# Optimization experiments

Measured on AMD Instinct MI355X. Metric: run time of the kernel, lower is better.

The kernel has to match this reference:

```python
import jax, jax.numpy as jnp
import numpy as np
import math

B, S, D, H = 4, 1024, 1024, 16
HD = D // H  # 64
DFF = 4 * D
LN_EPS = 1e-5

def setup_inputs() -> dict:
    key = jax.random.key(0)
    ks = jax.random.split(key, 24)
    sd = lambda fi, fo: 1.0 / math.sqrt(fi)
    def lin(k, fi, fo):
        k1, k2 = jax.random.split(k)
        w = jax.random.uniform(k1, (fi, fo), jnp.float32, -sd(fi, fo), sd(fi, fo))
        b = jax.random.uniform(k2, (fo,), jnp.float32, -sd(fi, fo), sd(fi, fo))
        return w, b
    x = jax.random.normal(ks[0], (B, S, D), jnp.float32)
    Wk, bk = lin(ks[1], D, D)
    Wq, bq = lin(ks[2], D, D)
    Wv, bv = lin(ks[3], D, D)
    # per-head projections stacked over heads: [H, D, HD]
    def head_lin(k):
        kk = jax.random.split(k, H)
        ws, bs = zip(*[lin(kk[h], D, HD) for h in range(H)])
        return jnp.stack(ws), jnp.stack(bs)
    Whq, bhq = head_lin(ks[4])
    Whk, bhk = head_lin(ks[5])
    Whv, bhv = head_lin(ks[6])
    Wo, bo = lin(ks[7], D, D)
    W1, b1 = lin(ks[8], D, DFF)
    W2, b2 = lin(ks[9], DFF, D)
    gamma = jnp.ones((D,), jnp.float32)
    beta = jnp.zeros((D,), jnp.float32)
    return dict(x=x, Wk=Wk, bk=bk, Wq=Wq, bq=bq, Wv=Wv, bv=bv,
                Whq=Whq, bhq=bhq, Whk=Whk, bhk=bhk, Whv=Whv, bhv=bhv,
                Wo=Wo, bo=bo, W1=W1, b1=b1, W2=W2, b2=b2,
                gamma=gamma, beta=beta)

def _layer_norm(x, gamma, beta):
    mu = jnp.mean(x, axis=-1, keepdims=True)
    var = jnp.mean(jnp.square(x - mu), axis=-1, keepdims=True)
    return (x - mu) * jax.lax.rsqrt(var + LN_EPS) * gamma + beta

def reference(x, Wk, bk, Wq, bq, Wv, bv, Whq, bhq, Whk, bhk, Whv, bhv,
              Wo, bo, W1, b1, W2, b2, gamma, beta):
    # outer projections; NOTE: forward passes (k, q, v) into MHA, so the
    # MHA 'Q' stream is k_proj(x), 'K' stream is q_proj(x), 'V' is v_proj(x)
    ko = x @ Wk + bk
    qo = x @ Wq + bq
    vo = x @ Wv + bv
    # per-head projections (batched over heads): [B,H,S,HD]
    q = jnp.einsum('bsd,hde->bhse', ko, Whq) + bhq[None, :, None, :]
    k = jnp.einsum('bsd,hde->bhse', qo, Whk) + bhk[None, :, None, :]
    v = jnp.einsum('bsd,hde->bhse', vo, Whv) + bhv[None, :, None, :]
    # NOTE: original scales by sqrt(d_model), not sqrt(head_dim)
    scores = jnp.einsum('bhse,bhte->bhst', q, k) / math.sqrt(D)
    w = jax.nn.softmax(scores, axis=-1)
    o = jnp.einsum('bhst,bhte->bhse', w, v)         # [B,H,S,HD]
    o = o.transpose(0, 2, 1, 3).reshape(B, S, D)    # concat heads
    attn = o @ Wo + bo
    # dropout is identity in eval; shared LayerNorm after both residuals
    r1 = _layer_norm(x + attn, gamma, beta)
    ff = jax.nn.gelu(r1 @ W1 + b1, approximate=False) @ W2 + b2
    out = _layer_norm(r1 + ff, gamma, beta)
    return out
```

## Files before the change

kernel.cpp:

```cpp
#include <hip/hip_runtime.h>
#include <cstdint>
#include <cstddef>

#define D_MODEL 1024
#define SEQ 1024
#define BATCH 4
#define NHEAD 16
#define HDIM 64
#define ROWS (BATCH*SEQ)

typedef unsigned short u16;
typedef __attribute__((ext_vector_type(4))) unsigned short u16x4;
typedef __attribute__((ext_vector_type(8))) unsigned short u16x8;
typedef __attribute__((ext_vector_type(8))) __bf16 bf16x8v;
typedef __attribute__((ext_vector_type(4))) float f32x4;

__device__ inline u16 f2bf(float f){
  union{float f; unsigned u;} c; c.f = f;
  unsigned r = c.u + 0x7FFFu + ((c.u>>16)&1u);
  return (u16)(r>>16);
}
__device__ inline float bf2f(u16 s){
  union{unsigned u; float f;} c; c.u = ((unsigned)s)<<16; return c.f;
}
__device__ inline float gelu_f(float x){ return 0.5f*x*(1.f+erff(x*0.7071067811865475f)); }

__device__ __forceinline__ void gload_lds16(const void* g, void* l){
  __builtin_amdgcn_global_load_lds(
    (const __attribute__((address_space(1))) unsigned int*)g,
    (__attribute__((address_space(3))) unsigned int*)l, 16, 0, 0);
}

struct C4 { const float* src[4]; u16* dst[4]; };
__global__ __launch_bounds__(256) void convert4(C4 p){
  int bid = blockIdx.x;
  int which, off;
  if (bid < 4096){ which = 0; off = bid; }
  else { which = 1 + ((bid-4096) >> 10); off = (bid-4096) & 1023; }
  size_t idx = (size_t)off*256 + threadIdx.x;
  f32x4 v = *(const f32x4*)(p.src[which] + idx*4);
  u16x4 o = { f2bf(v.x), f2bf(v.y), f2bf(v.z), f2bf(v.w) };
  *(u16x4*)(p.dst[which] + idx*4) = o;
}

struct T3 { const float* W[3]; u16* WT[3]; };
__global__ __launch_bounds__(256) void transpose3(T3 p){
  __shared__ float tile[32][33];
  int bid = blockIdx.x;
  int which, bx, by, K, N;
  if (bid < 1024){ which=0; K=1024; N=1024; bx=bid&31;  by=bid>>5; }
  else if (bid < 5120){ int i=bid-1024; which=1; K=1024; N=4096; bx=i&127; by=i>>7; }
  else { int i=bid-5120; which=2; K=4096; N=1024; bx=i&31; by=i>>5; }
  const float* W = p.W[which];
  u16* WT = p.WT[which];
  int n0 = bx*32, k0 = by*32;
  int tx = threadIdx.x & 31, ty = threadIdx.x >> 5;
  #pragma unroll
  for (int i=0;i<4;i++){
    int r = ty + i*8;
    tile[r][tx] = W[(size_t)(k0+r)*N + n0 + tx];
  }
  __syncthreads();
  #pragma unroll
  for (int i=0;i<4;i++){
    int r = ty + i*8;
    WT[(size_t)(n0+r)*K + k0 + tx] = f2bf(tile[tx][r]);
  }
}

struct H3 { const float* src[3]; u16* dst[3]; };
__global__ __launch_bounds__(256) void head_transpose3(H3 p){
  __shared__ float tile[32][33];
  int z = blockIdx.z; int which = z >> 4; int h = z & 15;
  const float* Wh = p.src[which];
  u16* WT = p.dst[which];
  int d0 = blockIdx.x*32, e0 = blockIdx.y*32;
  int tx = threadIdx.x & 31, ty = threadIdx.x >> 5;
  #pragma unroll
  for (int i=0;i<4;i++){
    int r = ty + i*8;
    tile[r][tx] = Wh[(size_t)h*D_MODEL*HDIM + (size_t)(d0+r)*HDIM + e0 + tx];
  }
  __syncthreads();
  #pragma unroll
  for (int i=0;i<4;i++){
    int r = ty + i*8;
    WT[(size_t)(h*HDIM + e0 + r)*D_MODEL + d0 + tx] = f2bf(tile[tx][r]);
  }
}

__global__ __launch_bounds__(64) void bias_comb(
  const float* bk, const float* bq, const float* bv,
  const float* Whq, const float* Whk, const float* Whv,
  const float* bhq, const float* bhk, const float* bhv, float* bc)
{
  int blk = blockIdx.x; int which = blk >> 4; int h = blk & 15; int e = threadIdx.x;
  const float* bvec = (which==0) ? bk : (which==1) ? bq : bv;
  const float* Wh   = (which==0) ? Whq : (which==1) ? Whk : Whv;
  const float* bh   = (which==0) ? bhq : (which==1) ? bhk : bhv;
  float s = bh[h*HDIM + e];
  const float* w = Wh + (size_t)h*D_MODEL*HDIM + e;
  for (int d=0; d<D_MODEL; ++d) s += bvec[d] * w[(size_t)d*HDIM];
  bc[which*1024 + h*HDIM + e] = s;
}

__global__ __launch_bounds__(512,1) void gemm256_8p(
  const u16* __restrict__ A, const u16* __restrict__ BT, const float* __restrict__ bias,
  u16* __restrict__ outB, int N, int K, int mode, int act)
{
  __shared__ __align__(16) u16 As[2][2][128*64];
  __shared__ __align__(16) u16 Bs[2][2][128*64];
  int t = threadIdx.x, lane = t&63, wid = t>>6;
  int wr = wid>>2, wc = wid&3;
  int fr = lane&15, kg = lane>>4;
  int gx = gridDim.x;
  int bid = blockIdx.y*gx + blockIdx.x;
  int nwg = gx*gridDim.y;
  int cpx = nwg>>3;
  int sw = (bid&7)*cpx + (bid>>3);
  int tc = sw % gx, tr = sw / gx;

  const u16* Abase = A  + (size_t)tr*256*K;
  const u16* Bbase = BT + (size_t)tc*256*K;
  int srow = lane>>3, sch8 = lane&7;

  f32x4 acc[8][4];
  #pragma unroll
  for (int m=0;m<8;m++)
    #pragma unroll
    for (int n=0;n<4;n++) acc[m][n] = (f32x4)0.f;

  bf16x8v af[2][4], bv0[2][2], bv1[2][2];

  #define STAGE_A8(buf,h,kt) { _Pragma("unroll") for (int li=0;li<2;li++){ \
    int sr = (wid*2+li)*8 + srow; \
    int gr = ((sr>>6)<<7) + (h)*64 + (sr&63); \
    int sc = sch8 ^ (sr&7); \
    gload_lds16(Abase + (size_t)gr*K + (size_t)(kt)*64 + sc*8, &As[buf][h][(wid*2+li)*512]); } }
  #define STAGE_B8(buf,h,kt) { _Pragma("unroll") for (int li=0;li<2;li++){ \
    int sr = (wid*2+li)*8 + srow; \
    int gc = ((sr>>5)<<6) + (h)*32 + (sr&31); \
    int sc = sch8 ^ (sr&7); \
    gload_lds16(Bbase + (size_t)gc*K + (size_t)(kt)*64 + sc*8, &Bs[buf][h][(wid*2+li)*512]); } }
  #define STAGE_ALL(buf,kt) { STAGE_A8(buf,0,kt); STAGE_B8(buf,0,kt); STAGE_B8(buf,1,kt); STAGE_A8(buf,1,kt); }
  #define LDA8(buf,h) { _Pragma("unroll") for (int ks=0;ks<2;ks++) _Pragma("unroll") for (int mf=0;mf<4;mf++){ \
    int r = wr*64 + mf*16 + fr; \
    af[ks][mf] = *(const bf16x8v*)&As[buf][h][r*64 + (((kg+4*ks)^(r&7)))*8]; } }
  #define LDB8(buf,h,dst) { _Pragma("unroll") for (int ks=0;ks<2;ks++) _Pragma("unroll") for (int nf=0;nf<2;nf++){ \
    int r = wc*32 + nf*16 + fr; \
    dst[ks][nf] = *(const bf16x8v*)&Bs[buf][h][r*64 + (((kg+4*ks)^(r&7)))*8]; } }
  #define MM8(mq,nq,bv) { asm volatile("s_waitcnt lgkmcnt(0)" ::: "memory"); \
    __builtin_amdgcn_s_setprio(1); \
    _Pragma("unroll") for (int ks=0;ks<2;ks++) _Pragma("unroll") for (int mf=0;mf<4;mf++) _Pragma("unroll") for (int nf=0;nf<2;nf++) \
      acc[(mq)*4+mf][(nq)*2+nf] = __builtin_amdgcn_mfma_f32_16x16x32_bf16(af[ks][mf], bv[ks][nf], acc[(mq)*4+mf][(nq)*2+nf], 0,0,0); \
    __builtin_amdgcn_s_setprio(0); }
  #define BAR asm volatile("s_barrier" ::: "memory")

  int NT = K >> 6;
  STAGE_ALL(0,0);

  for (int kt=0; kt<NT; ++kt){
    int buf = kt&1, nb = buf^1;
    if (kt+1 < NT){
      STAGE_ALL(nb, kt+1);
      asm volatile("s_waitcnt vmcnt(8)" ::: "memory");
    } else {
      asm volatile("s_waitcnt vmcnt(0)" ::: "memory");
    }
    BAR;
    LDA8(buf,0); LDB8(buf,0,bv0); MM8(0,0,bv0);
    LDB8(buf,1,bv1);              MM8(0,1,bv1);
    LDA8(buf,1);                  MM8(1,1,bv1);
                                  MM8(1,0,bv0);
  }

  int crow0 = tr*256 + wr*128;
  int ccol0 = tc*256 + wc*64;
  #pragma unroll
  for (int n=0;n<4;n++){
    int col = ccol0 + n*16 + fr;
    float bv = bias[col];
    #pragma unroll
    for (int m=0;m<8;m++){
      int rbase = crow0 + m*16 + kg*4;
      #pragma unroll
      for (int i=0;i<4;i++){
        float v = acc[m][n][i] + bv;
        if (act) v = gelu_f(v);
        int row = rbase + i;
        if (mode == 1){
          outB[(size_t)row*N + col] = f2bf(v);
        } else {
          int panel = col >> 10, c1 = col & 1023;
          if (panel < 2)
            outB[(size_t)panel*((size_t)ROWS*1024) + (size_t)row*1024 + c1] = f2bf(v);
          else {
            int b = row >> 10, s = row & 1023;
            int hh = c1 >> 6, e = c1 & 63;
            outB[(size_t)2*((size_t)ROWS*1024) + (((size_t)((b*NHEAD+hh)*HDIM+e))<<10) + s] = f2bf(v);
          }
        }
      }
    }
  }
}

__device__ __forceinline__ void stage128(u16 (*As)[4096], u16 (*Bs)[4096], int b,
  const u16* Ab, const u16* Bb, int Kstride, int kt, int wid, int rr, int sch)
{
  #pragma unroll
  for (int c=0;c<2;c++){
    int reg = c*4 + wid;
    int row = reg*16 + rr;
    gload_lds16(Ab + (size_t)row*Kstride + kt*32 + sch*8, &As[b][reg*512]);
  }
  #pragma unroll
  for (int c=0;c<2;c++){
    int reg = c*4 + wid;
    int row = reg*16 + rr;
    gload_lds16(Bb + (size_t)row*Kstride + kt*32 + sch*8, &Bs[b][reg*512]);
  }
}

__device__ __forceinline__ void gemm128_core(u16 (*As)[4096], u16 (*Bs)[4096],
  const u16* __restrict__ A, const u16* __restrict__ BT, const float* __restrict__ bias,
  float* __restrict__ outF, u16* __restrict__ outB,
  int N, int Kstride, int kofs, int Ksub, int mode, int act, int addbias)
{
  int t = threadIdx.x, lane = t&63, wid = t>>6;
  int wr = wid>>1, wc = wid&1;
  int fr = lane&15, kg = lane>>4;
  int gx = gridDim.x;
  int bid = blockIdx.y*gx + blockIdx.x;
  int nwg = gx*gridDim.y;
  int cpx = nwg >> 3;
  int sw = (bid&7)*cpx + (bid>>3);
  int tc = sw % gx, tr = sw / gx;

  const u16* Ab = A  + (size_t)tr*128*Kstride + kofs;
  const u16* Bb = BT + (size_t)tc*128*Kstride + kofs;
  int rr = lane>>2, cc = lane&3;
  int sch = cc ^ ((rr>>1)&3);

  f32x4 acc[4][4];
  #pragma unroll
  for (int m=0;m<4;m++)
    #pragma unroll
    for (int n=0;n<4;n++) acc[m][n] = (f32x4)0.f;

  int NT = Ksub >> 5;

  stage128(As, Bs, 0, Ab, Bb, Kstride, 0, wid, rr, sch);
  stage128(As, Bs, 1, Ab, Bb, Kstride, 1, wid, rr, sch);
  int buf = 0;
  for (int kt=0; kt<NT; ++kt){
    if (kt+2 < NT){
      int nb = buf+2; if (nb>=3) nb-=3;
      stage128(As, Bs, nb, Ab, Bb, Kstride, kt+2, wid, rr, sch);
      asm volatile("s_waitcnt vmcnt(8)" ::: "memory");
    } else if (kt+1 < NT){
      asm volatile("s_waitcnt vmcnt(4)" ::: "memory");
    } else {
      asm volatile("s_waitcnt vmcnt(0)" ::: "memory");
    }
    asm volatile("s_barrier" ::: "memory");
    bf16x8v af[4], bfv[4];
    #pragma unroll
    for (int m=0;m<4;m++){
      int r = wr*64 + m*16 + fr;
      af[m] = *(const bf16x8v*)&As[buf][r*32 + (kg ^ ((r>>1)&3))*8];
    }
    #pragma unroll
    for (int n=0;n<4;n++){
      int r = wc*64 + n*16 + fr;
      bfv[n] = *(const bf16x8v*)&Bs[buf][r*32 + (kg ^ ((r>>1)&3))*8];
    }
    #pragma unroll
    for (int m=0;m<4;m++)
      #pragma unroll
      for (int n=0;n<4;n++)
        acc[m][n] = __builtin_amdgcn_mfma_f32_16x16x32_bf16(af[m], bfv[n], acc[m][n], 0,0,0);
    if (kt+1 < NT)
      asm volatile("s_barrier" ::: "memory");
    buf += 1; if (buf >= 3) buf = 0;
  }

  int crow0 = tr*128 + wr*64;
  int ccol0 = tc*128 + wc*64;
  #pragma unroll
  for (int n=0;n<4;n++){
    int col = ccol0 + n*16 + fr;
    float bv = addbias ? bias[col] : 0.f;
    #pragma unroll
    for (int m=0;m<4;m++){
      int rbase = crow0 + m*16 + kg*4;
      #pragma unroll
      for (int i=0;i<4;i++){
        float v = acc[m][n][i] + bv;
        if (act) v = gelu_f(v);
        int row = rbase + i;
        if (mode == 1){
          outB[(size_t)row*N + col] = f2bf(v);
        } else {
          outF[(size_t)row*1024 + col] = v;
        }
      }
    }
  }
}

__global__ __launch_bounds__(256) void g_gemm_sk(
  const u16* A, const u16* BT, const float* bias, float* outBase, int K)
{
  __shared__ __align__(16) u16 As[3][4096];
  __shared__ __align__(16) u16 Bs[3][4096];
  int z = blockIdx.z;
  int Ksub = K >> 1;
  gemm128_core(As, Bs, A, BT, bias, outBase + (size_t)z*ROWS*1024, nullptr,
               1024, K, z*Ksub, Ksub, 3, 0, z==0);
}

struct B3 { const u16* A[3]; const u16* BT[3]; u16* Cb[3]; };
__global__ __launch_bounds__(256) void g_gemm_b3(B3 p, const float* bias){
  __shared__ __align__(16) u16 As[3][4096];
  __shared__ __align__(16) u16 Bs[3][4096];
  int z = blockIdx.z;
  gemm128_core(As, Bs, p.A[z], p.BT[z], bias, nullptr, p.Cb[z],
               1024, 1024, 0, 1024, 1, 0, 0);
}

__global__ __launch_bounds__(256) void attn_mfma(const u16* __restrict__ Q, const u16* __restrict__ Km,
                                                 const u16* __restrict__ Vt, u16* __restrict__ O)
{
  __shared__ __align__(16) u16 Ks[64*64];
  __shared__ __align__(16) u16 Vs[64*64];
  __shared__ __align__(16) u16 Ps[4][16*64];
  int t = threadIdx.x, lane = t & 63, wid = t >> 6;
  int fr = lane & 15, kg = lane >> 4;
  int qt = blockIdx.x, h = blockIdx.y, b = blockIdx.z;
  const size_t qkbase = ((size_t)b*SEQ)*D_MODEL + (size_t)h*HDIM;
  const size_t vtb = ((size_t)(b*NHEAD + h))*HDIM*SEQ;

  int qrow = qt*64 + wid*16 + fr;
  bf16x8v aq0 = *(const bf16x8v*)(Q + qkbase + (size_t)qrow*D_MODEL + kg*8);
  bf16x8v aq1 = *(const bf16x8v*)(Q + qkbase + (size_t)qrow*D_MODEL + 32 + kg*8);

  f32x4 Oacc[4];
  #pragma unroll
  for (int n=0;n<4;n++) Oacc[n] = (f32x4)0.f;
  float m_run[4], l_run[4];
  #pragma unroll
  for (int i=0;i<4;i++){ m_run[i] = -3e38f; l_run[i] = 0.f; }

  int srow = lane >> 3;
  int sch  = (lane & 7) ^ srow;
  int x7 = fr & 7;
  const float CS = 0.03125f * 1.4426950408889634f;
  u16* Pw = &Ps[wid][0];

  for (int kt = 0; kt < SEQ/64; ++kt){
    __syncthreads();
    #pragma unroll
    for (int c=0;c<2;c++){
      int r0 = (wid*2 + c)*8;
      int rowk = r0 + srow;
      gload_lds16(Km + qkbase + (size_t)(kt*64 + rowk)*D_MODEL + sch*8, &Ks[r0*64]);
      gload_lds16(Vt + vtb + (size_t)rowk*SEQ + kt*64 + sch*8, &Vs[r0*64]);
    }
    asm volatile("s_waitcnt vmcnt(0)" ::: "memory");
    __syncthreads();

    f32x4 s4[4];
    #pragma unroll
    for (int n=0;n<4;n++){
      int r = n*16 + fr;
      bf16x8v k0 = *(const bf16x8v*)&Ks[r*64 + ((kg  ) ^ x7)*8];
      bf16x8v k1 = *(const bf16x8v*)&Ks[r*64 + ((4+kg) ^ x7)*8];
      f32x4 z = (f32x4)0.f;
      z = __builtin_amdgcn_mfma_f32_16x16x32_bf16(aq0, k0, z, 0,0,0);
      s4[n] = __builtin_amdgcn_mfma_f32_16x16x32_bf16(aq1, k1, z, 0,0,0);
    }
    #pragma unroll
    for (int n=0;n<4;n++) s4[n] *= CS;

    float mI[4];
    #pragma unroll
    for (int i=0;i<4;i++)
      mI[i] = fmaxf(fmaxf(s4[0][i], s4[1][i]), fmaxf(s4[2][i], s4[3][i]));
    #pragma unroll
    for (int off=1; off<16; off<<=1){
      #pragma unroll
      for (int i=0;i<4;i++) mI[i] = fmaxf(mI[i], __shfl_xor(mI[i], off));
    }
    float g = -3e38f;
    #pragma unroll
    for (int i=0;i<4;i++) g = fmaxf(g, mI[i] - m_run[i]);
    if (__any(g > 8.f)){
      #pragma unroll
      for (int i=0;i<4;i++){
        float mn = fmaxf(m_run[i], mI[i]);
        float sc = exp2f(m_run[i] - mn);
        m_run[i] = mn;
        l_run[i] *= sc;
        #pragma unroll
        for (int n=0;n<4;n++) Oacc[n][i] *= sc;
      }
    }
    float ls[4] = {0.f,0.f,0.f,0.f};
    #pragma unroll
    for (int n=0;n<4;n++){
      int chunk = n*2 + (fr>>3);
      #pragma unroll
      for (int i=0;i<4;i++){
        float pv = exp2f(s4[n][i] - m_run[i]);
        ls[i] += pv;
        int row = kg*4 + i;
        Pw[row*64 + (chunk ^ (row&7))*8 + (fr&7)] = f2bf(pv);
      }
    }
    #pragma unroll
    for (int off=1; off<16; off<<=1){
      #pragma unroll
      for (int i=0;i<4;i++) ls[i] += __shfl_xor(ls[i], off);
    }
    #pragma unroll
    for (int i=0;i<4;i++) l_run[i] += ls[i];
    asm volatile("s_waitcnt lgkmcnt(0)" ::: "memory");

    bf16x8v ap0 = *(const bf16x8v*)&Pw[fr*64 + ((kg  ) ^ x7)*8];
    bf16x8v ap1 = *(const bf16x8v*)&Pw[fr*64 + ((4+kg) ^ x7)*8];
    #pragma unroll
    for (int n2=0;n2<4;n2++){
      int r = n2*16 + fr;
      bf16x8v v0 = *(const bf16x8v*)&Vs[r*64 + ((kg  ) ^ x7)*8];
      bf16x8v v1 = *(const bf16x8v*)&Vs[r*64 + ((4+kg) ^ x7)*8];
      Oacc[n2] = __builtin_amdgcn_mfma_f32_16x16x32_bf16(ap0, v0, Oacc[n2], 0,0,0);
      Oacc[n2] = __builtin_amdgcn_mfma_f32_16x16x32_bf16(ap1, v1, Oacc[n2], 0,0,0);
    }
  }

  float inv[4];
  #pragma unroll
  for (int i=0;i<4;i++) inv[i] = 1.f / l_run[i];
  #pragma unroll
  for (int n2=0;n2<4;n2++){
    #pragma unroll
    for (int i=0;i<4;i++){
      int row = qt*64 + wid*16 + kg*4 + i;
      O[qkbase + (size_t)row*D_MODEL + n2*16 + fr] = f2bf(Oacc[n2][i]*inv[i]);
    }
  }
}

__global__ __launch_bounds__(256) void ln_sum3(const float* __restrict__ A, const float* __restrict__ B,
   const float* __restrict__ C, const float* __restrict__ gamma, const float* __restrict__ beta,
   float* __restrict__ Of, u16* __restrict__ Ob)
{
  int row = blockIdx.x, t = threadIdx.x;
  size_t base = (size_t)row*D_MODEL + t*4;
  f32x4 v = *(const f32x4*)(A + base);
  v += *(const f32x4*)(B + base);
  v += *(const f32x4*)(C + base);
  float s = v.x+v.y+v.z+v.w;
  float q = v.x*v.x+v.y*v.y+v.z*v.z+v.w*v.w;
  #pragma unroll
  for (int off=1; off<64; off<<=1){ s += __shfl_xor(s,off); q += __shfl_xor(q,off); }
  __shared__ float red[8];
  int wid = t>>6;
  if ((t&63)==0){ red[wid] = s; red[wid+4] = q; }
  __syncthreads();
  s = red[0]+red[1]+red[2]+red[3];
  q = red[4]+red[5]+red[6]+red[7];
  float mu = s*(1.f/1024.f);
  float var = q*(1.f/1024.f) - mu*mu;
  float rs = rsqrtf(var + 1e-5f);
  f32x4 g4 = *(const f32x4*)(gamma + t*4);
  f32x4 b4 = *(const f32x4*)(beta + t*4);
  f32x4 o;
  o.x = (v.x-mu)*rs*g4.x + b4.x;
  o.y = (v.y-mu)*rs*g4.y + b4.y;
  o.z = (v.z-mu)*rs*g4.z + b4.z;
  o.w = (v.w-mu)*rs*g4.w + b4.w;
  if (Of) *(f32x4*)(Of + base) = o;
  if (Ob){
    u16x4 ob = { f2bf(o.x), f2bf(o.y), f2bf(o.z), f2bf(o.w) };
    *(u16x4*)(Ob + base) = ob;
  }
}

extern "C" void kernel_launch(void* const* d_in, const int* in_sizes, int n_in,
                              void* d_out, int out_size, void* d_ws, size_t ws_size,
                              hipStream_t stream)
{
  const float* x    = (const float*)d_in[0];
  const float* Wk   = (const float*)d_in[1];
  const float* bk   = (const float*)d_in[2];
  const float* Wq   = (const float*)d_in[3];
  const float* bq   = (const float*)d_in[4];
  const float* Wv   = (const float*)d_in[5];
  const float* bv   = (const float*)d_in[6];
  const float* Whq  = (const float*)d_in[7];
  const float* bhq  = (const float*)d_in[8];
  const float* Whk  = (const float*)d_in[9];
  const float* bhk  = (const float*)d_in[10];
  const float* Whv  = (const float*)d_in[11];
  const float* bhv  = (const float*)d_in[12];
  const float* Wo   = (const float*)d_in[13];
  const float* bo   = (const float*)d_in[14];
  const float* W1   = (const float*)d_in[15];
  const float* b1   = (const float*)d_in[16];
  const float* W2   = (const float*)d_in[17];
  const float* b2   = (const float*)d_in[18];
  const float* gamma= (const float*)d_in[19];
  const float* beta = (const float*)d_in[20];

  char* ws = (char*)d_ws;
  const size_t MB_ = 1024*1024;
  u16* Wkb  = (u16*)(ws + 0*MB_);
  u16* Wqb  = (u16*)(ws + 2*MB_);
  u16* Wvb  = (u16*)(ws + 4*MB_);
  u16* WhqT = (u16*)(ws + 6*MB_);
  u16* WhkT = (u16*)(ws + 8*MB_);
  u16* WhvT = (u16*)(ws + 10*MB_);
  u16* WoT  = (u16*)(ws + 12*MB_);
  u16* W1T  = (u16*)(ws + 14*MB_);
  u16* W2T  = (u16*)(ws + 22*MB_);
  u16* xb   = (u16*)(ws + 30*MB_);
  u16* WcT  = (u16*)(ws + 38*MB_);
  float* bc = (float*)(ws + 44*MB_);
  u16* qb   = (u16*)(ws + 46*MB_);
  u16* kb   = (u16*)(ws + 54*MB_);
  u16* vt   = (u16*)(ws + 62*MB_);
  u16* Ob   = (u16*)(ws + 70*MB_);
  float* Pa = (float*)(ws + 78*MB_);
  float* Pb = (float*)(ws + 94*MB_);
  float* r1f = (float*)(ws + 110*MB_);
  u16*  r1b  = (u16*)(ws + 38*MB_);
  u16*  ff1b = (u16*)(ws + 46*MB_);

  dim3 tb(256);

  C4 cv; cv.src[0]=x; cv.src[1]=Wk; cv.src[2]=Wq; cv.src[3]=Wv;
  cv.dst[0]=xb; cv.dst[1]=Wkb; cv.dst[2]=Wqb; cv.dst[3]=Wvb;
  convert4<<<dim3(4096+3072), tb, 0, stream>>>(cv);
  H3 hh; hh.src[0]=Whq; hh.src[1]=Whk; hh.src[2]=Whv;
  hh.dst[0]=WhqT; hh.dst[1]=WhkT; hh.dst[2]=WhvT;
  head_transpose3<<<dim3(32,2,48), tb, 0, stream>>>(hh);
  T3 tt; tt.W[0]=Wo; tt.W[1]=W1; tt.W[2]=W2;
  tt.WT[0]=WoT; tt.WT[1]=W1T; tt.WT[2]=W2T;
  transpose3<<<dim3(9216), tb, 0, stream>>>(tt);
  bias_comb<<<dim3(48), dim3(64), 0, stream>>>(bk,bq,bv, Whq,Whk,Whv, bhq,bhk,bhv, bc);

  B3 cmb;
  cmb.A[0]=WhqT; cmb.A[1]=WhkT; cmb.A[2]=WhvT;
  cmb.BT[0]=Wkb; cmb.BT[1]=Wqb; cmb.BT[2]=Wvb;
  cmb.Cb[0]=WcT; cmb.Cb[1]=WcT+1048576; cmb.Cb[2]=WcT+2097152;
  g_gemm_b3<<<dim3(8,8,3), tb, 0, stream>>>(cmb, bk);

  gemm256_8p<<<dim3(12,16), dim3(512), 0, stream>>>(xb, WcT, bc, qb, 3072, 1024, 2, 0);

  attn_mfma<<<dim3(16,16,4), tb, 0, stream>>>(qb, kb, vt, Ob);

  g_gemm_sk<<<dim3(8,32,2), tb, 0, stream>>>(Ob, WoT, bo, Pa, 1024);
  ln_sum3<<<dim3(4096), tb, 0, stream>>>(x, Pa, Pb, gamma, beta, r1f, r1b);
  gemm256_8p<<<dim3(16,16), dim3(512), 0, stream>>>(r1b, W1T, b1, ff1b, 4096, 1024, 1, 1);
  g_gemm_sk<<<dim3(8,32,2), tb, 0, stream>>>(ff1b, W2T, b2, Pa, 4096);
  ln_sum3<<<dim3(4096), tb, 0, stream>>>(r1f, Pa, Pb, gamma, beta, (float*)d_out, nullptr);

  (void)in_sizes; (void)n_in; (void)out_size; (void)ws_size;
}
```

Baseline: 333.0 us.

## Merge weight prep kernels, parallelize bias combine, defer softmax row-sum reduction

Folds the input conversion, weight transposes and per-head transposes into one prep_all launch, removing two kernel launches. bias_comb now uses 256 threads, splitting the 1024-long dot product into four segments reduced through shared memory. In attention, the per-tile cross-lane shuffle reduction of the softmax denominator moves out of the loop to a single reduction at the end, and P is rounded to bf16 with a cheaper round-half-up conversion that gives slightly different results on ties.

```diff
diff --git a/kernel.cpp b/kernel.cpp
--- a/kernel.cpp
+++ b/kernel.cpp
@@ -20,6 +20,10 @@
   unsigned r = c.u + 0x7FFFu + ((c.u>>16)&1u);
   return (u16)(r>>16);
 }
+__device__ inline u16 f2bf_fast(float f){
+  union{float f; unsigned u;} c; c.f = f;
+  return (u16)((c.u + 0x8000u)>>16);
+}
 __device__ inline float bf2f(u16 s){
   union{unsigned u; float f;} c; c.u = ((unsigned)s)<<16; return c.f;
 }
@@ -31,28 +35,39 @@
     (__attribute__((address_space(3))) unsigned int*)l, 16, 0, 0);
 }
 
-struct C4 { const float* src[4]; u16* dst[4]; };
-__global__ __launch_bounds__(256) void convert4(C4 p){
+struct PrepAll {
+  const float* conv_src[4]; u16* conv_dst[4];
+  const float* tr_src[3];   u16* tr_dst[3];
+  const float* h_src[3];    u16* h_dst[3];
+};
+__global__ __launch_bounds__(256) void prep_all(PrepAll p){
   int bid = blockIdx.x;
-  int which, off;
-  if (bid < 4096){ which = 0; off = bid; }
-  else { which = 1 + ((bid-4096) >> 10); off = (bid-4096) & 1023; }
-  size_t idx = (size_t)off*256 + threadIdx.x;
-  f32x4 v = *(const f32x4*)(p.src[which] + idx*4);
-  u16x4 o = { f2bf(v.x), f2bf(v.y), f2bf(v.z), f2bf(v.w) };
-  *(u16x4*)(p.dst[which] + idx*4) = o;
-}
-
-struct T3 { const float* W[3]; u16* WT[3]; };
-__global__ __launch_bounds__(256) void transpose3(T3 p){
+  if (bid < 7168){
+    int which, off;
+    if (bid < 4096){ which = 0; off = bid; }
+    else { which = 1 + ((bid-4096) >> 10); off = (bid-4096) & 1023; }
+    size_t idx = (size_t)off*256 + threadIdx.x;
+    f32x4 v = *(const f32x4*)(p.conv_src[which] + idx*4);
+    u16x4 o = { f2bf(v.x), f2bf(v.y), f2bf(v.z), f2bf(v.w) };
+    *(u16x4*)(p.conv_dst[which] + idx*4) = o;
+    return;
+  }
   __shared__ float tile[32][33];
-  int bid = blockIdx.x;
-  int which, bx, by, K, N;
-  if (bid < 1024){ which=0; K=1024; N=1024; bx=bid&31;  by=bid>>5; }
-  else if (bid < 5120){ int i=bid-1024; which=1; K=1024; N=4096; bx=i&127; by=i>>7; }
-  else { int i=bid-5120; which=2; K=4096; N=1024; bx=i&31; by=i>>5; }
-  const float* W = p.W[which];
-  u16* WT = p.WT[which];
+  bid -= 7168;
+  const float* W; u16* WT; int K, N, bx, by;
+  if (bid < 1024){ W=p.tr_src[0]; WT=p.tr_dst[0]; K=1024; N=1024; bx=bid&31; by=bid>>5; }
+  else if (bid < 5120){ int i=bid-1024; W=p.tr_src[1]; WT=p.tr_dst[1]; K=1024; N=4096; bx=i&127; by=i>>7; }
+  else if (bid < 9216){ int i=bid-5120; W=p.tr_src[2]; WT=p.tr_dst[2]; K=4096; N=1024; bx=i&31; by=i>>5; }
+  else {
+    int i = bid - 9216;
+    int which = i >> 10;
+    int j = i & 1023;
+    int h = j >> 6;
+    int d0t = (j>>1)&31, e0t = j&1;
+    W  = p.h_src[which] + (size_t)h*D_MODEL*HDIM;
+    WT = p.h_dst[which] + (size_t)h*HDIM*D_MODEL;
+    K = 1024; N = 64; bx = e0t; by = d0t;
+  }
   int n0 = bx*32, k0 = by*32;
   int tx = threadIdx.x & 31, ty = threadIdx.x >> 5;
   #pragma unroll
@@ -68,40 +83,26 @@
   }
 }
 
-struct H3 { const float* src[3]; u16* dst[3]; };
-__global__ __launch_bounds__(256) void head_transpose3(H3 p){
-  __shared__ float tile[32][33];
-  int z = blockIdx.z; int which = z >> 4; int h = z & 15;
-  const float* Wh = p.src[which];
-  u16* WT = p.dst[which];
-  int d0 = blockIdx.x*32, e0 = blockIdx.y*32;
-  int tx = threadIdx.x & 31, ty = threadIdx.x >> 5;
-  #pragma unroll
-  for (int i=0;i<4;i++){
-    int r = ty + i*8;
-    tile[r][tx] = Wh[(size_t)h*D_MODEL*HDIM + (size_t)(d0+r)*HDIM + e0 + tx];
-  }
-  __syncthreads();
-  #pragma unroll
-  for (int i=0;i<4;i++){
-    int r = ty + i*8;
-    WT[(size_t)(h*HDIM + e0 + r)*D_MODEL + d0 + tx] = f2bf(tile[tx][r]);
-  }
-}
-
-__global__ __launch_bounds__(64) void bias_comb(
+__global__ __launch_bounds__(256) void bias_comb(
   const float* bk, const float* bq, const float* bv,
   const float* Whq, const float* Whk, const float* Whv,
   const float* bhq, const float* bhk, const float* bhv, float* bc)
 {
-  int blk = blockIdx.x; int which = blk >> 4; int h = blk & 15; int e = threadIdx.x;
+  int blk = blockIdx.x; int which = blk >> 4; int h = blk & 15;
+  int e = threadIdx.x & 63, seg = threadIdx.x >> 6;
   const float* bvec = (which==0) ? bk : (which==1) ? bq : bv;
   const float* Wh   = (which==0) ? Whq : (which==1) ? Whk : Whv;
   const float* bh   = (which==0) ? bhq : (which==1) ? bhk : bhv;
-  float s = bh[h*HDIM + e];
   const float* w = Wh + (size_t)h*D_MODEL*HDIM + e;
-  for (int d=0; d<D_MODEL; ++d) s += bvec[d] * w[(size_t)d*HDIM];
-  bc[which*1024 + h*HDIM + e] = s;
+  float s = 0.f;
+  for (int d = seg*256; d < seg*256+256; ++d) s += bvec[d] * w[(size_t)d*HDIM];
+  __shared__ float red[256];
+  red[threadIdx.x] = s;
+  __syncthreads();
+  if (seg == 0){
+    s = red[e] + red[e+64] + red[e+128] + red[e+192] + bh[h*HDIM + e];
+    bc[which*1024 + h*HDIM + e] = s;
+  }
 }
 
 __global__ __launch_bounds__(512,1) void gemm256_8p(
@@ -406,25 +407,17 @@
         for (int n=0;n<4;n++) Oacc[n][i] *= sc;
       }
     }
-    float ls[4] = {0.f,0.f,0.f,0.f};
     #pragma unroll
     for (int n=0;n<4;n++){
       int chunk = n*2 + (fr>>3);
       #pragma unroll
       for (int i=0;i<4;i++){
         float pv = exp2f(s4[n][i] - m_run[i]);
-        ls[i] += pv;
+        l_run[i] += pv;
         int row = kg*4 + i;
-        Pw[row*64 + (chunk ^ (row&7))*8 + (fr&7)] = f2bf(pv);
+        Pw[row*64 + (chunk ^ (row&7))*8 + (fr&7)] = f2bf_fast(pv);
       }
     }
-    #pragma unroll
-    for (int off=1; off<16; off<<=1){
-      #pragma unroll
-      for (int i=0;i<4;i++) ls[i] += __shfl_xor(ls[i], off);
-    }
-    #pragma unroll
-    for (int i=0;i<4;i++) l_run[i] += ls[i];
     asm volatile("s_waitcnt lgkmcnt(0)" ::: "memory");
 
     bf16x8v ap0 = *(const bf16x8v*)&Pw[fr*64 + ((kg  ) ^ x7)*8];
@@ -439,6 +432,11 @@
     }
   }
 
+  #pragma unroll
+  for (int off=1; off<16; off<<=1){
+    #pragma unroll
+    for (int i=0;i<4;i++) l_run[i] += __shfl_xor(l_run[i], off);
+  }
   float inv[4];
   #pragma unroll
   for (int i=0;i<4;i++) inv[i] = 1.f / l_run[i];
@@ -540,16 +538,15 @@
 
   dim3 tb(256);
 
-  C4 cv; cv.src[0]=x; cv.src[1]=Wk; cv.src[2]=Wq; cv.src[3]=Wv;
-  cv.dst[0]=xb; cv.dst[1]=Wkb; cv.dst[2]=Wqb; cv.dst[3]=Wvb;
-  convert4<<<dim3(4096+3072), tb, 0, stream>>>(cv);
-  H3 hh; hh.src[0]=Whq; hh.src[1]=Whk; hh.src[2]=Whv;
-  hh.dst[0]=WhqT; hh.dst[1]=WhkT; hh.dst[2]=WhvT;
-  head_transpose3<<<dim3(32,2,48), tb, 0, stream>>>(hh);
-  T3 tt; tt.W[0]=Wo; tt.W[1]=W1; tt.W[2]=W2;
-  tt.WT[0]=WoT; tt.WT[1]=W1T; tt.WT[2]=W2T;
-  transpose3<<<dim3(9216), tb, 0, stream>>>(tt);
-  bias_comb<<<dim3(48), dim3(64), 0, stream>>>(bk,bq,bv, Whq,Whk,Whv, bhq,bhk,bhv, bc);
+  PrepAll pa;
+  pa.conv_src[0]=x;  pa.conv_src[1]=Wk; pa.conv_src[2]=Wq; pa.conv_src[3]=Wv;
+  pa.conv_dst[0]=xb; pa.conv_dst[1]=Wkb; pa.conv_dst[2]=Wqb; pa.conv_dst[3]=Wvb;
+  pa.tr_src[0]=Wo;  pa.tr_src[1]=W1;  pa.tr_src[2]=W2;
+  pa.tr_dst[0]=WoT; pa.tr_dst[1]=W1T; pa.tr_dst[2]=W2T;
+  pa.h_src[0]=Whq;  pa.h_src[1]=Whk;  pa.h_src[2]=Whv;
+  pa.h_dst[0]=WhqT; pa.h_dst[1]=WhkT; pa.h_dst[2]=WhvT;
+  prep_all<<<dim3(19456), tb, 0, stream>>>(pa);
+  bias_comb<<<dim3(48), tb, 0, stream>>>(bk,bq,bv, Whq,Whk,Whv, bhq,bhk,bhv, bc);
 
   B3 cmb;
   cmb.A[0]=WhqT; cmb.A[1]=WhkT; cmb.A[2]=WhvT;
```

Result: slower. 356.7 us (+7.1%).

## Restructure big GEMM to K=32 tiles, parallelize bias_comb, defer attention row-sum reduction

Applied to the files above, without the earlier changes.

The 256x256 bf16 GEMM now stages K=32 slices (32 KB LDS instead of 128 KB) with a new XOR swizzle, a simpler single-phase MFMA loop and launch bounds allowing more resident blocks, trading twice as many barrier iterations for smaller LDS use. bias_comb splits the 1024-long dot product across four waves with a shared-memory reduction. Attention keeps per-lane partial row sums and does the cross-lane shuffle reduction once at the end instead of every key tile. It also uses a cheaper round-half-up bf16 conversion for the probabilities, which changes rounding slightly.

```diff
diff --git a/kernel.cpp b/kernel.cpp
--- a/kernel.cpp
+++ b/kernel.cpp
@@ -19,6 +19,10 @@
   union{float f; unsigned u;} c; c.f = f;
   unsigned r = c.u + 0x7FFFu + ((c.u>>16)&1u);
   return (u16)(r>>16);
+}
+__device__ inline u16 f2bf_fast(float f){
+  union{float f; unsigned u;} c; c.f = f;
+  return (u16)((c.u + 0x8000u)>>16);
 }
 __device__ inline float bf2f(u16 s){
   union{unsigned u; float f;} c; c.u = ((unsigned)s)<<16; return c.f;
@@ -89,27 +93,34 @@
   }
 }
 
-__global__ __launch_bounds__(64) void bias_comb(
+__global__ __launch_bounds__(256) void bias_comb(
   const float* bk, const float* bq, const float* bv,
   const float* Whq, const float* Whk, const float* Whv,
   const float* bhq, const float* bhk, const float* bhv, float* bc)
 {
-  int blk = blockIdx.x; int which = blk >> 4; int h = blk & 15; int e = threadIdx.x;
+  int blk = blockIdx.x; int which = blk >> 4; int h = blk & 15;
+  int e = threadIdx.x & 63, seg = threadIdx.x >> 6;
   const float* bvec = (which==0) ? bk : (which==1) ? bq : bv;
   const float* Wh   = (which==0) ? Whq : (which==1) ? Whk : Whv;
   const float* bh   = (which==0) ? bhq : (which==1) ? bhk : bhv;
-  float s = bh[h*HDIM + e];
   const float* w = Wh + (size_t)h*D_MODEL*HDIM + e;
-  for (int d=0; d<D_MODEL; ++d) s += bvec[d] * w[(size_t)d*HDIM];
-  bc[which*1024 + h*HDIM + e] = s;
-}
-
-__global__ __launch_bounds__(512,1) void gemm256_8p(
+  float s = 0.f;
+  for (int d = seg*256; d < seg*256+256; ++d) s += bvec[d] * w[(size_t)d*HDIM];
+  __shared__ float red[256];
+  red[threadIdx.x] = s;
+  __syncthreads();
+  if (seg == 0){
+    s = red[e] + red[e+64] + red[e+128] + red[e+192] + bh[h*HDIM + e];
+    bc[which*1024 + h*HDIM + e] = s;
+  }
+}
+
+__global__ __launch_bounds__(512,4) void gemm256b(
   const u16* __restrict__ A, const u16* __restrict__ BT, const float* __restrict__ bias,
   u16* __restrict__ outB, int N, int K, int mode, int act)
 {
-  __shared__ __align__(16) u16 As[2][2][128*64];
-  __shared__ __align__(16) u16 Bs[2][2][128*64];
+  __shared__ __align__(16) u16 As[2][256*32];
+  __shared__ __align__(16) u16 Bs[2][256*32];
   int t = threadIdx.x, lane = t&63, wid = t>>6;
   int wr = wid>>2, wc = wid&3;
   int fr = lane&15, kg = lane>>4;
@@ -122,7 +133,7 @@
 
   const u16* Abase = A  + (size_t)tr*256*K;
   const u16* Bbase = BT + (size_t)tc*256*K;
-  int srow = lane>>3, sch8 = lane&7;
+  int rr4 = lane>>2, cc4 = lane&3;
 
   f32x4 acc[8][4];
   #pragma unroll
@@ -130,48 +141,46 @@
     #pragma unroll
     for (int n=0;n<4;n++) acc[m][n] = (f32x4)0.f;
 
-  bf16x8v af[2][4], bv0[2][2], bv1[2][2];
-
-  #define STAGE_A8(buf,h,kt) { _Pragma("unroll") for (int li=0;li<2;li++){ \
-    int sr = (wid*2+li)*8 + srow; \
-    int gr = ((sr>>6)<<7) + (h)*64 + (sr&63); \
-    int sc = sch8 ^ (sr&7); \
-    gload_lds16(Abase + (size_t)gr*K + (size_t)(kt)*64 + sc*8, &As[buf][h][(wid*2+li)*512]); } }
-  #define STAGE_B8(buf,h,kt) { _Pragma("unroll") for (int li=0;li<2;li++){ \
-    int sr = (wid*2+li)*8 + srow; \
-    int gc = ((sr>>5)<<6) + (h)*32 + (sr&31); \
-    int sc = sch8 ^ (sr&7); \
-    gload_lds16(Bbase + (size_t)gc*K + (size_t)(kt)*64 + sc*8, &Bs[buf][h][(wid*2+li)*512]); } }
-  #define STAGE_ALL(buf,kt) { STAGE_A8(buf,0,kt); STAGE_B8(buf,0,kt); STAGE_B8(buf,1,kt); STAGE_A8(buf,1,kt); }
-  #define LDA8(buf,h) { _Pragma("unroll") for (int ks=0;ks<2;ks++) _Pragma("unroll") for (int mf=0;mf<4;mf++){ \
-    int r = wr*64 + mf*16 + fr; \
-    af[ks][mf] = *(const bf16x8v*)&As[buf][h][r*64 + (((kg+4*ks)^(r&7)))*8]; } }
-  #define LDB8(buf,h,dst) { _Pragma("unroll") for (int ks=0;ks<2;ks++) _Pragma("unroll") for (int nf=0;nf<2;nf++){ \
-    int r = wc*32 + nf*16 + fr; \
-    dst[ks][nf] = *(const bf16x8v*)&Bs[buf][h][r*64 + (((kg+4*ks)^(r&7)))*8]; } }
-  #define MM8(mq,nq,bv) { asm volatile("s_waitcnt lgkmcnt(0)" ::: "memory"); \
-    __builtin_amdgcn_s_setprio(1); \
-    _Pragma("unroll") for (int ks=0;ks<2;ks++) _Pragma("unroll") for (int mf=0;mf<4;mf++) _Pragma("unroll") for (int nf=0;nf<2;nf++) \
-      acc[(mq)*4+mf][(nq)*2+nf] = __builtin_amdgcn_mfma_f32_16x16x32_bf16(af[ks][mf], bv[ks][nf], acc[(mq)*4+mf][(nq)*2+nf], 0,0,0); \
-    __builtin_amdgcn_s_setprio(0); }
-  #define BAR asm volatile("s_barrier" ::: "memory")
-
-  int NT = K >> 6;
-  STAGE_ALL(0,0);
-
+  #define STG(buf,kt) { _Pragma("unroll") for (int ri=0;ri<2;ri++){ \
+      int sr = ri*128 + wid*16 + rr4; \
+      int sc = cc4 ^ ((sr>>1)&3); \
+      gload_lds16(Abase + (size_t)sr*K + (size_t)(kt)*32 + sc*8, &As[buf][(ri*128 + wid*16)*32]); } \
+    _Pragma("unroll") for (int ri=0;ri<2;ri++){ \
+      int sr = ri*128 + wid*16 + rr4; \
+      int sc = cc4 ^ ((sr>>1)&3); \
+      gload_lds16(Bbase + (size_t)sr*K + (size_t)(kt)*32 + sc*8, &Bs[buf][(ri*128 + wid*16)*32]); } }
+
+  int NT = K >> 5;
+  STG(0,0);
   for (int kt=0; kt<NT; ++kt){
-    int buf = kt&1, nb = buf^1;
+    int buf = kt&1;
     if (kt+1 < NT){
-      STAGE_ALL(nb, kt+1);
-      asm volatile("s_waitcnt vmcnt(8)" ::: "memory");
+      STG(buf^1, kt+1);
+      asm volatile("s_waitcnt vmcnt(4)" ::: "memory");
     } else {
       asm volatile("s_waitcnt vmcnt(0)" ::: "memory");
     }
-    BAR;
-    LDA8(buf,0); LDB8(buf,0,bv0); MM8(0,0,bv0);
-    LDB8(buf,1,bv1);              MM8(0,1,bv1);
-    LDA8(buf,1);                  MM8(1,1,bv1);
-                                  MM8(1,0,bv0);
+    asm volatile("s_barrier" ::: "memory");
+    bf16x8v af[8], bfv[4];
+    #pragma unroll
+    for (int mf=0;mf<8;mf++){
+      int r = wr*128 + mf*16 + fr;
+      af[mf] = *(const bf16x8v*)&As[buf][r*32 + (kg ^ ((r>>1)&3))*8];
+    }
+    #pragma unroll
+    for (int nf=0;nf<4;nf++){
+      int r = wc*64 + nf*16 + fr;
+      bfv[nf] = *(const bf16x8v*)&Bs[buf][r*32 + (kg ^ ((r>>1)&3))*8];
+    }
+    __builtin_amdgcn_s_setprio(1);
+    #pragma unroll
+    for (int mf=0;mf<8;mf++)
+      #pragma unroll
+      for (int nf=0;nf<4;nf++)
+        acc[mf][nf] = __builtin_amdgcn_mfma_f32_16x16x32_bf16(af[mf], bfv[nf], acc[mf][nf], 0,0,0);
+    __builtin_amdgcn_s_setprio(0);
+    if (kt+1 < NT)
+      asm volatile("s_barrier" ::: "memory");
   }
 
   int crow0 = tr*256 + wr*128;
@@ -406,25 +415,17 @@
         for (int n=0;n<4;n++) Oacc[n][i] *= sc;
       }
     }
-    float ls[4] = {0.f,0.f,0.f,0.f};
     #pragma unroll
     for (int n=0;n<4;n++){
       int chunk = n*2 + (fr>>3);
       #pragma unroll
       for (int i=0;i<4;i++){
         float pv = exp2f(s4[n][i] - m_run[i]);
-        ls[i] += pv;
+        l_run[i] += pv;
         int row = kg*4 + i;
-        Pw[row*64 + (chunk ^ (row&7))*8 + (fr&7)] = f2bf(pv);
+        Pw[row*64 + (chunk ^ (row&7))*8 + (fr&7)] = f2bf_fast(pv);
       }
     }
-    #pragma unroll
-    for (int off=1; off<16; off<<=1){
-      #pragma unroll
-      for (int i=0;i<4;i++) ls[i] += __shfl_xor(ls[i], off);
-    }
-    #pragma unroll
-    for (int i=0;i<4;i++) l_run[i] += ls[i];
     asm volatile("s_waitcnt lgkmcnt(0)" ::: "memory");
 
     bf16x8v ap0 = *(const bf16x8v*)&Pw[fr*64 + ((kg  ) ^ x7)*8];
@@ -439,6 +440,11 @@
     }
   }
 
+  #pragma unroll
+  for (int off=1; off<16; off<<=1){
+    #pragma unroll
+    for (int i=0;i<4;i++) l_run[i] += __shfl_xor(l_run[i], off);
+  }
   float inv[4];
   #pragma unroll
   for (int i=0;i<4;i++) inv[i] = 1.f / l_run[i];
@@ -549,7 +555,7 @@
   T3 tt; tt.W[0]=Wo; tt.W[1]=W1; tt.W[2]=W2;
   tt.WT[0]=WoT; tt.WT[1]=W1T; tt.WT[2]=W2T;
   transpose3<<<dim3(9216), tb, 0, stream>>>(tt);
-  bias_comb<<<dim3(48), dim3(64), 0, stream>>>(bk,bq,bv, Whq,Whk,Whv, bhq,bhk,bhv, bc);
+  bias_comb<<<dim3(48), tb, 0, stream>>>(bk,bq,bv, Whq,Whk,Whv, bhq,bhk,bhv, bc);
 
   B3 cmb;
   cmb.A[0]=WhqT; cmb.A[1]=WhkT; cmb.A[2]=WhvT;
@@ -557,13 +563,13 @@
   cmb.Cb[0]=WcT; cmb.Cb[1]=WcT+1048576; cmb.Cb[2]=WcT+2097152;
   g_gemm_b3<<<dim3(8,8,3), tb, 0, stream>>>(cmb, bk);
 
-  gemm256_8p<<<dim3(12,16), dim3(512), 0, stream>>>(xb, WcT, bc, qb, 3072, 1024, 2, 0);
+  gemm256b<<<dim3(12,16), dim3(512), 0, stream>>>(xb, WcT, bc, qb, 3072, 1024, 2, 0);
 
   attn_mfma<<<dim3(16,16,4), tb, 0, stream>>>(qb, kb, vt, Ob);
 
   g_gemm_sk<<<dim3(8,32,2), tb, 0, stream>>>(Ob, WoT, bo, Pa, 1024);
   ln_sum3<<<dim3(4096), tb, 0, stream>>>(x, Pa, Pb, gamma, beta, r1f, r1b);
-  gemm256_8p<<<dim3(16,16), dim3(512), 0, stream>>>(r1b, W1T, b1, ff1b, 4096, 1024, 1, 1);
+  gemm256b<<<dim3(16,16), dim3(512), 0, stream>>>(r1b, W1T, b1, ff1b, 4096, 1024, 1, 1);
   g_gemm_sk<<<dim3(8,32,2), tb, 0, stream>>>(ff1b, W2T, b2, Pa, 4096);
   ln_sum3<<<dim3(4096), tb, 0, stream>>>(r1f, Pa, Pb, gamma, beta, (float*)d_out, nullptr);
 
```

New measurement: 935.0 us. 181% more time.
